# Kernel tuning notes

Measured on AMD Instinct MI355X. Metric: run time of the kernel, lower is better.

## Reference

```python
import jax, jax.numpy as jnp
import numpy as np

N, E = 100000, 800000
D_IN, D_HID, D_OUT = 128, 128, 40


def _lin_params(key, d_out, d_in, bias):
    k1, k2 = jax.random.split(key)
    bound = 1.0 / np.sqrt(d_in)
    W = jax.random.uniform(k1, (d_out, d_in), jnp.float32, -bound, bound)
    if bias:
        b = jax.random.uniform(k2, (d_out,), jnp.float32, -bound, bound)
        return W, b
    return W


def setup_inputs() -> dict:
    key = jax.random.key(0)
    ks = jax.random.split(key, 8)
    x = jax.random.normal(ks[0], (N, D_IN), jnp.float32)
    edge_index = jax.random.randint(ks[1], (2, E), 0, N, jnp.int64)
    Wl0, b0 = _lin_params(ks[2], D_HID, D_IN, True)
    Wr0 = _lin_params(ks[3], D_HID, D_IN, False)
    Wl1, b1 = _lin_params(ks[4], D_HID, D_HID, True)
    Wr1 = _lin_params(ks[5], D_HID, D_HID, False)
    Wl2, b2 = _lin_params(ks[6], D_OUT, D_HID, True)
    Wr2 = _lin_params(ks[7], D_OUT, D_HID, False)
    return {"x": x, "edge_index": edge_index,
            "Wl0": Wl0, "Wr0": Wr0, "b0": b0,
            "Wl1": Wl1, "Wr1": Wr1, "b1": b1,
            "Wl2": Wl2, "Wr2": Wr2, "b2": b2}


def _sage_conv(x, src, dst, Wl, Wr, b):
    # mean aggregation of neighbor messages (src -> dst), PyG SAGEConv semantics
    msg = x[src]                                               # [E, d]
    agg = jax.ops.segment_sum(msg, dst, num_segments=N)        # [N, d]
    deg = jax.ops.segment_sum(jnp.ones((src.shape[0],), x.dtype), dst,
                              num_segments=N)                  # [N]
    agg = agg / jnp.maximum(deg, 1.0)[:, None]
    # out = lin_l(agg) + lin_r(x); lin_l has bias, lin_r does not
    return agg @ Wl.T + x @ Wr.T + b


def reference(x, edge_index, Wl0, Wr0, b0, Wl1, Wr1, b1, Wl2, Wr2, b2):
    src, dst = edge_index[0], edge_index[1]
    h = jax.nn.relu(_sage_conv(x, src, dst, Wl0, Wr0, b0))   # dropout = identity in eval
    h = jax.nn.relu(_sage_conv(h, src, dst, Wl1, Wr1, b1))
    h = _sage_conv(h, src, dst, Wl2, Wr2, b2)
    return jax.nn.log_softmax(h, axis=1)
```

## Files before the change

kernel.cpp:

```cpp
#include <hip/hip_runtime.h>
#include <hip/hip_bf16.h>
#include <math.h>

#define D 128
typedef unsigned int uint;
typedef unsigned short ushort;

using bf16x8 = __attribute__((ext_vector_type(8))) short;
using f32x4  = __attribute__((ext_vector_type(4))) float;
using f32x2  = __attribute__((ext_vector_type(2))) float;

static __device__ __forceinline__ ushort f2b(float f) {
    __hip_bfloat16 h = __float2bfloat16(f);
    return __builtin_bit_cast(ushort, h);
}
static __device__ __forceinline__ float blo(uint u) {
    uint v = u << 16;
    return __builtin_bit_cast(float, v);
}
static __device__ __forceinline__ float bhi(uint u) {
    uint v = u & 0xFFFF0000u;
    return __builtin_bit_cast(float, v);
}

#define NBLK_A 1024
#define MAXB   128
#define WTOT   (2*128*256 + 80*128)

__global__ __launch_bounds__(256) void k_bcount(
    const int* __restrict__ dst, int* __restrict__ cnt, int E, int nbuck,
    const float* __restrict__ x, ushort* __restrict__ Abuf, int n4,
    const float* __restrict__ Wl0, const float* __restrict__ Wr0,
    const float* __restrict__ Wl1, const float* __restrict__ Wr1,
    const float* __restrict__ Wl2, const float* __restrict__ Wr2,
    ushort* __restrict__ Wtg0, ushort* __restrict__ Wtg1,
    ushort* __restrict__ W2tg)
{
    __shared__ int h[MAXB];
    int tid = threadIdx.x, b = blockIdx.x;
    for (int k = tid; k < nbuck; k += 256) h[k] = 0;
    __syncthreads();
    int chunk = (E + NBLK_A - 1) / NBLK_A;
    int beg = b * chunk, end = min(beg + chunk, E);
    for (int e = beg + tid; e < end; e += 256)
        atomicAdd(&h[dst[e] >> 10], 1);
    __syncthreads();
    for (int k = tid; k < nbuck; k += 256) cnt[k * NBLK_A + b] = h[k];

    for (int i = b * 256 + tid; i < n4; i += NBLK_A * 256) {
        float4 v = *(const float4*)(x + (size_t)i * 4);
        int node = i >> 5, coff = (i & 31) * 4;
        ushort4 o;
        o.x = f2b(v.x); o.y = f2b(v.y); o.z = f2b(v.z); o.w = f2b(v.w);
        *(ushort4*)(Abuf + (size_t)node * 256 + 128 + coff) = o;
    }
    for (int i = b * 256 + tid; i < WTOT; i += NBLK_A * 256) {
        if (i < 2 * 128 * 256) {
            int which = i >> 15;
            int o = i & 32767;
            int j = o >> 8, kk = o & 255;
            const float* Wl = which ? Wl1 : Wl0;
            const float* Wr = which ? Wr1 : Wr0;
            float v = (kk < 128) ? Wl[j * 128 + kk] : Wr[j * 128 + (kk - 128)];
            (which ? Wtg1 : Wtg0)[o] = f2b(v);
        } else {
            int o = i - 2 * 128 * 256;
            int j = o >> 7, kk = o & 127;
            float v = (j < 40) ? Wl2[j * 128 + kk] : Wr2[(j - 40) * 128 + kk];
            W2tg[o] = f2b(v);
        }
    }
}

__global__ __launch_bounds__(256) void k_scanA(int* __restrict__ a,
                                               int* __restrict__ bsum, int n) {
    __shared__ int s[256];
    int tid = threadIdx.x;
    int i = blockIdx.x * 256 + tid;
    int v = (i < n) ? a[i] : 0;
    s[tid] = v;
    __syncthreads();
#pragma unroll
    for (int o = 1; o < 256; o <<= 1) {
        int t = (tid >= o) ? s[tid - o] : 0;
        __syncthreads();
        s[tid] += t;
        __syncthreads();
    }
    if (i < n) a[i] = s[tid] - v;
    if (tid == 255) bsum[blockIdx.x] = s[255];
}

__global__ void k_scan2(int* __restrict__ bsum, int nb,
                        int* __restrict__ bb, int nbuck, int E) {
    __shared__ int s[512];
    __shared__ int carry_s;
    int tid = threadIdx.x;
    if (tid == 0) carry_s = 0;
    __syncthreads();
    for (int base = 0; base < nb; base += 512) {
        int i = base + tid;
        int v = (i < nb) ? bsum[i] : 0;
        s[tid] = v;
        __syncthreads();
#pragma unroll
        for (int o = 1; o < 512; o <<= 1) {
            int t = (tid >= o) ? s[tid - o] : 0;
            __syncthreads();
            s[tid] += t;
            __syncthreads();
        }
        int carry = carry_s;
        if (i < nb) bsum[i] = s[tid] - v + carry;
        int total = s[511];
        __syncthreads();
        if (tid == 0) carry_s = carry + total;
        __syncthreads();
    }
    for (int k = tid; k < nbuck; k += 512) bb[k] = bsum[k * (NBLK_A >> 8)];
    if (tid == 0) bb[nbuck] = E;
}

__global__ __launch_bounds__(256) void k_bplace(
    const int* __restrict__ src, const int* __restrict__ dst,
    const int* __restrict__ cnt, const int* __restrict__ bsum,
    uint* __restrict__ ebuf, int E, int nbuck)
{
    __shared__ int cur[MAXB];
    int tid = threadIdx.x, b = blockIdx.x;
    for (int k = tid; k < nbuck; k += 256) {
        int idx = k * NBLK_A + b;
        cur[k] = cnt[idx] + bsum[idx >> 8];
    }
    __syncthreads();
    int chunk = (E + NBLK_A - 1) / NBLK_A;
    int beg = b * chunk, end = min(beg + chunk, E);
    for (int e = beg + tid; e < end; e += 256) {
        int d = dst[e];
        int r = atomicAdd(&cur[d >> 10], 1);
        ebuf[r] = (uint)src[e] | ((uint)(d & 1023) << 20);
    }
}

__global__ __launch_bounds__(1024) void k_bfine(
    const uint* __restrict__ ebuf, const int* __restrict__ bb,
    int* __restrict__ rowptr, int* __restrict__ col, int nN, int nbuck, int E)
{
    __shared__ int cnt2[1024];
    __shared__ int sc[1024];
    int k = blockIdx.x, tid = threadIdx.x;
    int e0 = bb[k], e1 = bb[k + 1];
    cnt2[tid] = 0;
    __syncthreads();
    for (int e = e0 + tid; e < e1; e += 1024)
        atomicAdd(&cnt2[ebuf[e] >> 20], 1);
    __syncthreads();
    int v = cnt2[tid];
    sc[tid] = v;
    __syncthreads();
#pragma unroll
    for (int o = 1; o < 1024; o <<= 1) {
        int t = (tid >= o) ? sc[tid - o] : 0;
        __syncthreads();
        sc[tid] += t;
        __syncthreads();
    }
    int excl = sc[tid] - v;
    int node = k * 1024 + tid;
    if (node < nN) rowptr[node] = e0 + excl;
    if (k == nbuck - 1 && tid == 0) rowptr[nN] = E;
    cnt2[tid] = e0 + excl;
    __syncthreads();
    for (int e = e0 + tid; e < e1; e += 1024) {
        uint sd = ebuf[e];
        int r = atomicAdd(&cnt2[sd >> 20], 1);
        col[r] = (int)(sd & 0xFFFFFu);
    }
}

__global__ __launch_bounds__(256) void k_gather128(
    const ushort* __restrict__ feat, ushort* __restrict__ agg,
    const int* __restrict__ rowptr, const int* __restrict__ col, int nN)
{
    int tid = threadIdx.x;
    int lane = tid & 63;
    int h = lane >> 5;
    int node = blockIdx.x * 8 + ((tid >> 6) << 1) + h;
    if (node >= nN) return;
    int g = (lane >> 4) & 1;
    int r = lane & 15;
    int beg = rowptr[node], end = rowptr[node + 1];
    const char* fb = (const char*)feat;
    const uint rb = (uint)(r << 4);
    float a[8];
#pragma unroll
    for (int i = 0; i < 8; ++i) a[i] = 0.f;

    int j = beg + g;
    for (; j + 2 < end; j += 4) {
        int s0 = col[j], s1 = col[j + 2];
        uint4 v0 = *(const uint4*)(fb + (((uint)s0 << 9) + rb));
        uint4 v1 = *(const uint4*)(fb + (((uint)s1 << 9) + rb));
        const uint* p0 = (const uint*)&v0;
        const uint* p1 = (const uint*)&v1;
#pragma unroll
        for (int i = 0; i < 4; ++i) {
            a[2 * i]     += blo(p0[i]) + blo(p1[i]);
            a[2 * i + 1] += bhi(p0[i]) + bhi(p1[i]);
        }
    }
    if (j < end) {
        int s0 = col[j];
        uint4 v0 = *(const uint4*)(fb + (((uint)s0 << 9) + rb));
        const uint* p0 = (const uint*)&v0;
#pragma unroll
        for (int i = 0; i < 4; ++i) {
            a[2 * i]     += blo(p0[i]);
            a[2 * i + 1] += bhi(p0[i]);
        }
    }
#pragma unroll
    for (int i = 0; i < 8; ++i)
        a[i] += __shfl_xor(a[i], 16);
    if (g == 0) {
        float inv = 1.0f / (float)max(end - beg, 1);
        uint4 o;
        uint* po = (uint*)&o;
#pragma unroll
        for (int i = 0; i < 4; ++i)
            po[i] = (uint)f2b(a[2 * i] * inv) | ((uint)f2b(a[2 * i + 1] * inv) << 16);
        *(uint4*)(agg + (size_t)node * 256 + r * 8) = o;
    }
}

template<int OUTJ, int KDIM, int SW, int MODE>
__global__ __launch_bounds__(256) void k_gemm_mfma(
    const ushort* __restrict__ A, int astride,
    const ushort* __restrict__ Wt, const float* __restrict__ bias,
    ushort* __restrict__ out, int ostride, ushort* __restrict__ out2, int nN)
{
    constexpr int NT = OUTJ / 16;
    constexpr int KSTEPS = KDIM / 32;
    __shared__ __align__(16) ushort Ws[OUTJ * SW];

    const int tid = threadIdx.x;
    constexpr int CHUNKS = OUTJ * KDIM / 8;
#pragma unroll
    for (int c = tid; c < CHUNKS; c += 256) {
        int row = c / (KDIM / 8);
        int ko  = (c % (KDIM / 8)) * 8;
        *(uint4*)(Ws + row * SW + ko) = *(const uint4*)(Wt + row * KDIM + ko);
    }
    __syncthreads();

    const int l = tid & 63, wv = tid >> 6;
    const int q = l >> 4, r = l & 15;
    const long long m0 = (long long)blockIdx.x * 128 + wv * 32;
    const int mA = (int)min(m0 + r, (long long)(nN - 1));
    const int mB = (int)min(m0 + 16 + r, (long long)(nN - 1));
    const ushort* pa = A + (size_t)mA * astride + q * 8;
    const ushort* pb = A + (size_t)mB * astride + q * 8;

    f32x4 acc[2][NT];
#pragma unroll
    for (int mt = 0; mt < 2; ++mt)
#pragma unroll
        for (int nt = 0; nt < NT; ++nt)
            acc[mt][nt] = (f32x4){0.f, 0.f, 0.f, 0.f};

    bf16x8 a0 = *(const bf16x8*)pa;
    bf16x8 a1 = *(const bf16x8*)pb;
#pragma unroll
    for (int ks = 0; ks < KSTEPS; ++ks) {
        bf16x8 a0n = a0, a1n = a1;
        if (ks + 1 < KSTEPS) {
            a0n = *(const bf16x8*)(pa + (ks + 1) * 32);
            a1n = *(const bf16x8*)(pb + (ks + 1) * 32);
        }
#pragma unroll
        for (int nt = 0; nt < NT; ++nt) {
            bf16x8 b = *(const bf16x8*)(Ws + (nt * 16 + r) * SW + ks * 32 + q * 8);
            acc[0][nt] = __builtin_amdgcn_mfma_f32_16x16x32_bf16(a0, b, acc[0][nt], 0, 0, 0);
            acc[1][nt] = __builtin_amdgcn_mfma_f32_16x16x32_bf16(a1, b, acc[1][nt], 0, 0, 0);
        }
        a0 = a0n; a1 = a1n;
    }

#pragma unroll
    for (int mt = 0; mt < 2; ++mt) {
#pragma unroll
        for (int i = 0; i < 4; ++i) {
            long long m = m0 + mt * 16 + q * 4 + i;
            if (m >= nN) continue;
#pragma unroll
            for (int nt = 0; nt < NT; ++nt) {
                int cc = nt * 16 + r;
                float v = acc[mt][nt][i];
                if (MODE == 0) {
                    v += bias[cc];
                    v = fmaxf(v, 0.f);
                    out[(size_t)m * ostride + cc] = f2b(v);
                } else {
                    if (cc < 40) out[(size_t)m * 40 + cc] = f2b(v);
                    else { v += bias[cc - 40]; out2[(size_t)m * 40 + (cc - 40)] = f2b(v); }
                }
            }
        }
    }
}

__global__ __launch_bounds__(256) void k_gather40_lsm(
    const ushort* __restrict__ P, const ushort* __restrict__ R,
    const int* __restrict__ rowptr, const int* __restrict__ col,
    float* __restrict__ out, int nN)
{
    int tid = threadIdx.x;
    int lane = tid & 63;
    int h = lane >> 4;
    int node = blockIdx.x * 16 + ((tid >> 6) << 2) + h;
    if (node >= nN) return;
    int g = (lane >> 3) & 1;
    int r = lane & 7;
    int beg = rowptr[node], end = rowptr[node + 1];
    const char* pbase = (const char*)P;
    const uint rb = (uint)(r << 4);
    f32x2 a2[4];
#pragma unroll
    for (int i = 0; i < 4; ++i) a2[i] = (f32x2){0.f, 0.f};

    int j = beg + g;
    for (; j + 2 < end; j += 4) {
        int s0 = col[j], s1 = col[j + 2];
        uint4 v0 = *(const uint4*)(pbase + ((((uint)s0 * 5u) << 4) + rb));
        uint4 v1 = *(const uint4*)(pbase + ((((uint)s1 * 5u) << 4) + rb));
        const uint* p0 = (const uint*)&v0;
        const uint* p1 = (const uint*)&v1;
#pragma unroll
        for (int i = 0; i < 4; ++i)
            a2[i] += (f32x2){blo(p0[i]) + blo(p1[i]), bhi(p0[i]) + bhi(p1[i])};
    }
    if (j < end) {
        int s0 = col[j];
        uint4 v0 = *(const uint4*)(pbase + ((((uint)s0 * 5u) << 4) + rb));
        const uint* p0 = (const uint*)&v0;
#pragma unroll
        for (int i = 0; i < 4; ++i)
            a2[i] += (f32x2){blo(p0[i]), bhi(p0[i])};
    }
    float a[8];
#pragma unroll
    for (int i = 0; i < 4; ++i) { a[2 * i] = a2[i].x; a[2 * i + 1] = a2[i].y; }
#pragma unroll
    for (int i = 0; i < 8; ++i)
        a[i] += __shfl_xor(a[i], 8);
    float inv = 1.0f / (float)max(end - beg, 1);
    uint4 rv = *(const uint4*)(R + (size_t)node * 40 + r * 8);
    const uint* pr = (const uint*)&rv;
    float vv[8];
    float mx = -INFINITY;
#pragma unroll
    for (int i = 0; i < 8; ++i) {
        float rc = (i & 1) ? bhi(pr[i >> 1]) : blo(pr[i >> 1]);
        int c = r * 8 + i;
        vv[i] = (c < 40) ? (a[i] * inv + rc) : -INFINITY;
        mx = fmaxf(mx, vv[i]);
    }
    mx = fmaxf(mx, __shfl_xor(mx, 1));
    mx = fmaxf(mx, __shfl_xor(mx, 2));
    mx = fmaxf(mx, __shfl_xor(mx, 4));
    float s = 0.f;
#pragma unroll
    for (int i = 0; i < 8; ++i) {
        int c = r * 8 + i;
        if (c < 40) s += __expf(vv[i] - mx);
    }
    s += __shfl_xor(s, 1);
    s += __shfl_xor(s, 2);
    s += __shfl_xor(s, 4);
    float lse = mx + __logf(s);
    if (g == 0 && r < 5) {
        float4 o0 = make_float4(vv[0] - lse, vv[1] - lse, vv[2] - lse, vv[3] - lse);
        float4 o1 = make_float4(vv[4] - lse, vv[5] - lse, vv[6] - lse, vv[7] - lse);
        *(float4*)(out + (size_t)node * 40 + r * 8)     = o0;
        *(float4*)(out + (size_t)node * 40 + r * 8 + 4) = o1;
    }
}

extern "C" void kernel_launch(void* const* d_in, const int* in_sizes, int n_in,
                              void* d_out, int out_size, void* d_ws, size_t ws_size,
                              hipStream_t stream) {
    const float* x   = (const float*)d_in[0];
    const int*   ei  = (const int*)d_in[1];
    const float* Wl0 = (const float*)d_in[2];
    const float* Wr0 = (const float*)d_in[3];
    const float* b0  = (const float*)d_in[4];
    const float* Wl1 = (const float*)d_in[5];
    const float* Wr1 = (const float*)d_in[6];
    const float* b1  = (const float*)d_in[7];
    const float* Wl2 = (const float*)d_in[8];
    const float* Wr2 = (const float*)d_in[9];
    const float* b2  = (const float*)d_in[10];
    const int nN = in_sizes[0] / D;
    const int E  = in_sizes[1] / 2;
    const int* src = ei;
    const int* dst = ei + E;

    char* w = (char*)d_ws;
    auto alloc = [&](size_t bytes) { char* p = w; w += (bytes + 255) & ~(size_t)255; return p; };
    const int nbuck = (nN + 1023) >> 10;
    const int ncnt  = nbuck * NBLK_A;
    int*    cnt    = (int*)   alloc((size_t)ncnt * 4);
    int*    bsum   = (int*)   alloc((size_t)((ncnt + 255) / 256) * 4);
    int*    bb     = (int*)   alloc((size_t)(nbuck + 1) * 4);
    int*    rowptr = (int*)   alloc((size_t)(nN + 1) * 4);
    int*    col    = (int*)   alloc((size_t)E * 4);
    ushort* AbufA  = (ushort*)alloc((size_t)nN * 256 * 2);
    ushort* AbufB  = (ushort*)alloc((size_t)nN * 256 * 2);
    ushort* Wtg0   = (ushort*)alloc((size_t)128 * 256 * 2);
    ushort* Wtg1   = (ushort*)alloc((size_t)128 * 256 * 2);
    ushort* W2tg   = (ushort*)alloc((size_t)80 * 128 * 2);
    uint*   ebuf   = (uint*)AbufB;
    ushort* Pbuf   = AbufB;
    ushort* Rbuf   = AbufB + (size_t)nN * 40;
    float*  logits = (float*)d_out;

    const int GATH_BLKS = (nN + 7) / 8;
    const int G40_BLKS  = (nN + 15) / 16;
    const int GEMM_BLKS = (nN + 127) / 128;
    const int n4        = nN * 32;
    const int NBSC      = (ncnt + 255) / 256;

    k_bcount<<<NBLK_A, 256, 0, stream>>>(dst, cnt, E, nbuck, x, AbufA, n4,
                                         Wl0, Wr0, Wl1, Wr1, Wl2, Wr2,
                                         Wtg0, Wtg1, W2tg);
    k_scanA <<<NBSC, 256, 0, stream>>>(cnt, bsum, ncnt);
    k_scan2 <<<1, 512, 0, stream>>>(bsum, NBSC, bb, nbuck, E);
    k_bplace<<<NBLK_A, 256, 0, stream>>>(src, dst, cnt, bsum, ebuf, E, nbuck);
    k_bfine <<<nbuck, 1024, 0, stream>>>(ebuf, bb, rowptr, col, nN, nbuck, E);

    k_gather128<<<GATH_BLKS, 256, 0, stream>>>(AbufA + 128, AbufA, rowptr, col, nN);
    k_gemm_mfma<128, 256, 264, 0><<<GEMM_BLKS, 256, 0, stream>>>(
        AbufA, 256, Wtg0, b0, AbufB + 128, 256, nullptr, nN);

    k_gather128<<<GATH_BLKS, 256, 0, stream>>>(AbufB + 128, AbufB, rowptr, col, nN);
    k_gemm_mfma<128, 256, 264, 0><<<GEMM_BLKS, 256, 0, stream>>>(
        AbufB, 256, Wtg1, b1, AbufA + 128, 256, nullptr, nN);

    k_gemm_mfma<80, 128, 136, 1><<<GEMM_BLKS, 256, 0, stream>>>(
        AbufA + 128, 256, W2tg, b2, Pbuf, 40, Rbuf, nN);
    k_gather40_lsm<<<G40_BLKS, 256, 0, stream>>>(Pbuf, Rbuf, rowptr, col, logits, nN);
}
```

Measured before the change: 294.4 us.

## Fuse layer-1 GEMM with layer-2 projection GEMM via shared memory

The second layer's GEMM now keeps its ReLU output tile in shared memory and immediately multiplies it by the third-layer weights. This removes one kernel launch and the round trip of writing and re-reading the 128-wide hidden activations from global memory. The P/R buffers move to AbufA because AbufB is now the fused kernel's input. The cost is a longer kernel with an extra barrier and a second weight load per block, and reusing the same shared buffer may affect occupancy.

```diff
diff --git a/kernel.cpp b/kernel.cpp
--- a/kernel.cpp
+++ b/kernel.cpp
@@ -233,23 +233,20 @@
     }
 }
 
-template<int OUTJ, int KDIM, int SW, int MODE>
 __global__ __launch_bounds__(256) void k_gemm_mfma(
     const ushort* __restrict__ A, int astride,
     const ushort* __restrict__ Wt, const float* __restrict__ bias,
-    ushort* __restrict__ out, int ostride, ushort* __restrict__ out2, int nN)
-{
-    constexpr int NT = OUTJ / 16;
-    constexpr int KSTEPS = KDIM / 32;
-    __shared__ __align__(16) ushort Ws[OUTJ * SW];
+    ushort* __restrict__ out, int ostride, int nN)
+{
+    constexpr int SW = 264;
+    __shared__ __align__(16) ushort Ws[128 * SW];
 
     const int tid = threadIdx.x;
-    constexpr int CHUNKS = OUTJ * KDIM / 8;
-#pragma unroll
-    for (int c = tid; c < CHUNKS; c += 256) {
-        int row = c / (KDIM / 8);
-        int ko  = (c % (KDIM / 8)) * 8;
-        *(uint4*)(Ws + row * SW + ko) = *(const uint4*)(Wt + row * KDIM + ko);
+#pragma unroll
+    for (int c = tid; c < 128 * 32; c += 256) {
+        int row = c >> 5;
+        int ko  = (c & 31) * 8;
+        *(uint4*)(Ws + row * SW + ko) = *(const uint4*)(Wt + row * 256 + ko);
     }
     __syncthreads();
 
@@ -261,24 +258,24 @@
     const ushort* pa = A + (size_t)mA * astride + q * 8;
     const ushort* pb = A + (size_t)mB * astride + q * 8;
 
-    f32x4 acc[2][NT];
+    f32x4 acc[2][8];
 #pragma unroll
     for (int mt = 0; mt < 2; ++mt)
 #pragma unroll
-        for (int nt = 0; nt < NT; ++nt)
+        for (int nt = 0; nt < 8; ++nt)
             acc[mt][nt] = (f32x4){0.f, 0.f, 0.f, 0.f};
 
     bf16x8 a0 = *(const bf16x8*)pa;
     bf16x8 a1 = *(const bf16x8*)pb;
 #pragma unroll
-    for (int ks = 0; ks < KSTEPS; ++ks) {
+    for (int ks = 0; ks < 8; ++ks) {
         bf16x8 a0n = a0, a1n = a1;
-        if (ks + 1 < KSTEPS) {
+        if (ks + 1 < 8) {
             a0n = *(const bf16x8*)(pa + (ks + 1) * 32);
             a1n = *(const bf16x8*)(pb + (ks + 1) * 32);
         }
 #pragma unroll
-        for (int nt = 0; nt < NT; ++nt) {
+        for (int nt = 0; nt < 8; ++nt) {
             bf16x8 b = *(const bf16x8*)(Ws + (nt * 16 + r) * SW + ks * 32 + q * 8);
             acc[0][nt] = __builtin_amdgcn_mfma_f32_16x16x32_bf16(a0, b, acc[0][nt], 0, 0, 0);
             acc[1][nt] = __builtin_amdgcn_mfma_f32_16x16x32_bf16(a1, b, acc[1][nt], 0, 0, 0);
@@ -293,17 +290,123 @@
             long long m = m0 + mt * 16 + q * 4 + i;
             if (m >= nN) continue;
 #pragma unroll
-            for (int nt = 0; nt < NT; ++nt) {
+            for (int nt = 0; nt < 8; ++nt) {
                 int cc = nt * 16 + r;
-                float v = acc[mt][nt][i];
-                if (MODE == 0) {
-                    v += bias[cc];
-                    v = fmaxf(v, 0.f);
-                    out[(size_t)m * ostride + cc] = f2b(v);
-                } else {
-                    if (cc < 40) out[(size_t)m * 40 + cc] = f2b(v);
-                    else { v += bias[cc - 40]; out2[(size_t)m * 40 + (cc - 40)] = f2b(v); }
-                }
+                float v = acc[mt][nt][i] + bias[cc];
+                v = fmaxf(v, 0.f);
+                out[(size_t)m * ostride + cc] = f2b(v);
+            }
+        }
+    }
+}
+
+__global__ __launch_bounds__(256) void k_gemm12(
+    const ushort* __restrict__ A,
+    const ushort* __restrict__ Wt1,
+    const float* __restrict__ b1,
+    const ushort* __restrict__ W2,
+    const float* __restrict__ b2,
+    ushort* __restrict__ P,
+    ushort* __restrict__ R,
+    int nN)
+{
+    constexpr int SW = 264, H2S = 140, W2S = 136, W2OFF = 128 * H2S;
+    __shared__ __align__(16) ushort Ws[128 * SW];
+
+    const int tid = threadIdx.x;
+#pragma unroll
+    for (int c = tid; c < 128 * 32; c += 256) {
+        int row = c >> 5;
+        int ko  = (c & 31) * 8;
+        *(uint4*)(Ws + row * SW + ko) = *(const uint4*)(Wt1 + row * 256 + ko);
+    }
+    __syncthreads();
+
+    const int l = tid & 63, wv = tid >> 6;
+    const int q = l >> 4, r = l & 15;
+    const long long m0 = (long long)blockIdx.x * 128 + wv * 32;
+    const int mA = (int)min(m0 + r, (long long)(nN - 1));
+    const int mB = (int)min(m0 + 16 + r, (long long)(nN - 1));
+    const ushort* pa = A + (size_t)mA * 256 + q * 8;
+    const ushort* pb = A + (size_t)mB * 256 + q * 8;
+
+    f32x4 acc[2][8];
+#pragma unroll
+    for (int mt = 0; mt < 2; ++mt)
+#pragma unroll
+        for (int nt = 0; nt < 8; ++nt)
+            acc[mt][nt] = (f32x4){0.f, 0.f, 0.f, 0.f};
+
+    bf16x8 a0 = *(const bf16x8*)pa;
+    bf16x8 a1 = *(const bf16x8*)pb;
+#pragma unroll
+    for (int ks = 0; ks < 8; ++ks) {
+        bf16x8 a0n = a0, a1n = a1;
+        if (ks + 1 < 8) {
+            a0n = *(const bf16x8*)(pa + (ks + 1) * 32);
+            a1n = *(const bf16x8*)(pb + (ks + 1) * 32);
+        }
+#pragma unroll
+        for (int nt = 0; nt < 8; ++nt) {
+            bf16x8 b = *(const bf16x8*)(Ws + (nt * 16 + r) * SW + ks * 32 + q * 8);
+            acc[0][nt] = __builtin_amdgcn_mfma_f32_16x16x32_bf16(a0, b, acc[0][nt], 0, 0, 0);
+            acc[1][nt] = __builtin_amdgcn_mfma_f32_16x16x32_bf16(a1, b, acc[1][nt], 0, 0, 0);
+        }
+        a0 = a0n; a1 = a1n;
+    }
+    __syncthreads();
+
+#pragma unroll
+    for (int mt = 0; mt < 2; ++mt)
+#pragma unroll
+        for (int i = 0; i < 4; ++i) {
+            int row = wv * 32 + mt * 16 + q * 4 + i;
+#pragma unroll
+            for (int nt = 0; nt < 8; ++nt) {
+                int cc = nt * 16 + r;
+                float v = acc[mt][nt][i] + b1[cc];
+                Ws[row * H2S + cc] = f2b(fmaxf(v, 0.f));
+            }
+        }
+#pragma unroll
+    for (int c = tid; c < 80 * 16; c += 256) {
+        int row = c >> 4;
+        int ko  = (c & 15) * 8;
+        *(uint4*)(Ws + W2OFF + row * W2S + ko) = *(const uint4*)(W2 + row * 128 + ko);
+    }
+    __syncthreads();
+
+    f32x4 acc2[2][5];
+#pragma unroll
+    for (int mt = 0; mt < 2; ++mt)
+#pragma unroll
+        for (int nt = 0; nt < 5; ++nt)
+            acc2[mt][nt] = (f32x4){0.f, 0.f, 0.f, 0.f};
+
+#pragma unroll
+    for (int ks = 0; ks < 4; ++ks) {
+        bf16x8 a0b = *(const bf16x8*)(Ws + (wv * 32 + r) * H2S + ks * 32 + q * 8);
+        bf16x8 a1b = *(const bf16x8*)(Ws + (wv * 32 + 16 + r) * H2S + ks * 32 + q * 8);
+#pragma unroll
+        for (int nt = 0; nt < 5; ++nt) {
+            bf16x8 b = *(const bf16x8*)(Ws + W2OFF + (nt * 16 + r) * W2S + ks * 32 + q * 8);
+            acc2[0][nt] = __builtin_amdgcn_mfma_f32_16x16x32_bf16(a0b, b, acc2[0][nt], 0, 0, 0);
+            acc2[1][nt] = __builtin_amdgcn_mfma_f32_16x16x32_bf16(a1b, b, acc2[1][nt], 0, 0, 0);
+        }
+    }
+
+#pragma unroll
+    for (int mt = 0; mt < 2; ++mt) {
+#pragma unroll
+        for (int i = 0; i < 4; ++i) {
+            long long m = m0 + mt * 16 + q * 4 + i;
+            if (m >= nN) continue;
+#pragma unroll
+            for (int nt = 0; nt < 5; ++nt) {
+                int cc = nt * 16 + r;
+                float v = acc2[mt][nt][i];
+                if (cc < 40) P[(size_t)m * 40 + cc] = f2b(v);
+                else { v += b2[cc - 40]; R[(size_t)m * 40 + (cc - 40)] = f2b(v); }
             }
         }
     }
@@ -420,8 +523,8 @@
     ushort* Wtg1   = (ushort*)alloc((size_t)128 * 256 * 2);
     ushort* W2tg   = (ushort*)alloc((size_t)80 * 128 * 2);
     uint*   ebuf   = (uint*)AbufB;
-    ushort* Pbuf   = AbufB;
-    ushort* Rbuf   = AbufB + (size_t)nN * 40;
+    ushort* Pbuf   = AbufA;
+    ushort* Rbuf   = AbufA + (size_t)nN * 40;
     float*  logits = (float*)d_out;
 
     const int GATH_BLKS = (nN + 7) / 8;
@@ -439,14 +542,12 @@
     k_bfine <<<nbuck, 1024, 0, stream>>>(ebuf, bb, rowptr, col, nN, nbuck, E);
 
     k_gather128<<<GATH_BLKS, 256, 0, stream>>>(AbufA + 128, AbufA, rowptr, col, nN);
-    k_gemm_mfma<128, 256, 264, 0><<<GEMM_BLKS, 256, 0, stream>>>(
-        AbufA, 256, Wtg0, b0, AbufB + 128, 256, nullptr, nN);
+    k_gemm_mfma<<<GEMM_BLKS, 256, 0, stream>>>(
+        AbufA, 256, Wtg0, b0, AbufB + 128, 256, nN);
 
     k_gather128<<<GATH_BLKS, 256, 0, stream>>>(AbufB + 128, AbufB, rowptr, col, nN);
-    k_gemm_mfma<128, 256, 264, 0><<<GEMM_BLKS, 256, 0, stream>>>(
-        AbufB, 256, Wtg1, b1, AbufA + 128, 256, nullptr, nN);
-
-    k_gemm_mfma<80, 128, 136, 1><<<GEMM_BLKS, 256, 0, stream>>>(
-        AbufA + 128, 256, W2tg, b2, Pbuf, 40, Rbuf, nN);
+    k_gemm12<<<GEMM_BLKS, 256, 0, stream>>>(
+        AbufB, Wtg1, b1, W2tg, b2, Pbuf, Rbuf, nN);
+
     k_gather40_lsm<<<G40_BLKS, 256, 0, stream>>>(Pbuf, Rbuf, rowptr, col, logits, nN);
 }
```

Result: faster. 286.4 us (median of 2 runs) (-2.7%).
